# Kernel optimization log

Hardware: AMD Instinct MI355X
Metric: run time of the kernel (lower is better)

The kernel has to match this reference:

```python
import jax, jax.numpy as jnp
import numpy as np

N, IN_F, OUT_F, HEADS = 50000, 128, 16, 4
HC = OUT_F * HEADS  # 64
E = 800000
BN_EPS = 1e-5
NEG_SLOPE = 0.2


def setup_inputs() -> dict:
    key = jax.random.key(0)
    ks = jax.random.split(key, 9)
    x = jax.random.normal(ks[0], (N, IN_F), dtype=jnp.float32)
    edge_index = jax.random.randint(ks[1], (2, E), 0, N, dtype=jnp.int64)
    W = jax.random.normal(ks[2], (IN_F, HC), dtype=jnp.float32) * (1.0 / np.sqrt(IN_F))
    a_src = jax.random.normal(ks[3], (HEADS, OUT_F), dtype=jnp.float32) * 0.1
    a_dst = jax.random.normal(ks[4], (HEADS, OUT_F), dtype=jnp.float32) * 0.1
    bias = jax.random.normal(ks[5], (HC,), dtype=jnp.float32) * 0.01
    gamma = jnp.ones((HC,), dtype=jnp.float32) + 0.1 * jax.random.normal(ks[6], (HC,), dtype=jnp.float32)
    beta = 0.1 * jax.random.normal(ks[7], (HC,), dtype=jnp.float32)
    W_res = jax.random.normal(ks[8], (IN_F, HC), dtype=jnp.float32) * (1.0 / np.sqrt(IN_F))
    return {"x": x, "edge_index": edge_index, "W": W, "a_src": a_src,
            "a_dst": a_dst, "bias": bias, "gamma": gamma, "beta": beta, "W_res": W_res}


def reference(x, edge_index, W, a_src, a_dst, bias, gamma, beta, W_res):
    n = x.shape[0]
    # GATConv adds self-loops by default
    loops = jnp.tile(jnp.arange(n, dtype=edge_index.dtype)[None, :], (2, 1))
    ei = jnp.concatenate([edge_index, loops], axis=1)
    src, dst = ei[0], ei[1]

    h = (x @ W).reshape(n, HEADS, OUT_F)  # [N,H,C]
    al_s = jnp.einsum('nhc,hc->nh', h, a_src)  # [N,H]
    al_d = jnp.einsum('nhc,hc->nh', h, a_dst)

    e = jax.nn.leaky_relu(al_s[src] + al_d[dst], NEG_SLOPE)  # [E,H]
    # per-destination segment softmax (self-loops guarantee non-empty segments)
    e_max = jax.lax.stop_gradient(jax.ops.segment_max(e, dst, num_segments=n))
    m = jnp.exp(e - e_max[dst])
    denom = jax.ops.segment_sum(m, dst, num_segments=n)  # [N,H]
    alpha = m / denom[dst]  # [E,H]

    # scatter-add weighted source features
    msg = alpha[:, :, None] * h[src]  # [E,H,C]
    out = jax.ops.segment_sum(msg, dst, num_segments=n).reshape(n, HC) + bias

    # BatchNorm (training mode: batch statistics over nodes) then ELU
    mu = out.mean(axis=0)
    var = out.var(axis=0)
    y = (out - mu) * jax.lax.rsqrt(var + BN_EPS) * gamma + beta
    y = jax.nn.elu(y)
    # dropout identity (eval); residual projection since in_feats != H*C
    return y + x @ W_res
```

## Files before the change

kernel.cpp:

```cpp
#include <hip/hip_runtime.h>
#include <hip/hip_bf16.h>

#define NN 50000
#define EE 800000
#define IN_F 128
#define HC 64
#define NEG_SLOPE 0.2f
#define BN_EPS 1e-5f

#define NBKT 196
#define NBLKS 200
#define EPB2 (EE / NBLKS)
#define TOTH (NBKT * NBLKS)
#define GEMM_BLOCKS 512
#define NTILES ((NN + 63) / 64)

typedef __attribute__((ext_vector_type(8))) short short8;
typedef __attribute__((ext_vector_type(4))) float f32x4;

__device__ __forceinline__ ushort f2bf(float f) {
  uint u = __float_as_uint(f);
  uint r = u + 0x7FFF + ((u >> 16) & 1);
  return (ushort)(r >> 16);
}
__device__ __forceinline__ float bf2f(ushort u) {
  return __uint_as_float(((uint)u) << 16);
}

__global__ __launch_bounds__(256) void gemm_mfma_kernel(
    const float* __restrict__ x, const float* __restrict__ W, const float* __restrict__ Wres,
    const float* __restrict__ a_src, const float* __restrict__ a_dst,
    ushort* __restrict__ h, ushort* __restrict__ res,
    float* __restrict__ al_s, float* __restrict__ al_d) {
  __shared__ ushort bs[128 * 128];
  __shared__ ushort xs[64 * 128];

  const int tid = threadIdx.x;

  {
    const int c4 = (tid & 31) * 4;
    const int kb = (tid >> 5) * 16;
    const float* src0 = (c4 < HC) ? (W + c4) : (Wres + (c4 - HC));
    char* base = (char*)bs;
#pragma unroll
    for (int j = 0; j < 8; ++j) {
      int k0 = kb + j * 2;
      float4 fa = *(const float4*)(src0 + (size_t)k0 * HC);
      float4 fb = *(const float4*)(src0 + (size_t)(k0 + 1) * HC);
      uint p0 = (uint)f2bf(fa.x) | ((uint)f2bf(fb.x) << 16);
      uint p1 = (uint)f2bf(fa.y) | ((uint)f2bf(fb.y) << 16);
      uint p2 = (uint)f2bf(fa.z) | ((uint)f2bf(fb.z) << 16);
      uint p3 = (uint)f2bf(fa.w) | ((uint)f2bf(fb.w) << 16);
      *(uint*)(base + (((c4 + 0) * 256 + k0 * 2) ^ (((c4 + 0) & 7) << 4))) = p0;
      *(uint*)(base + (((c4 + 1) * 256 + k0 * 2) ^ (((c4 + 1) & 7) << 4))) = p1;
      *(uint*)(base + (((c4 + 2) * 256 + k0 * 2) ^ (((c4 + 2) & 7) << 4))) = p2;
      *(uint*)(base + (((c4 + 3) * 256 + k0 * 2) ^ (((c4 + 3) & 7) << 4))) = p3;
    }
  }

  const int w = tid >> 6;
  const int l = tid & 63;
  const int lr = l & 15;
  const int lk = (l >> 4) * 8;
  const char* xb = (const char*)xs;
  const char* bb = (const char*)bs;
  const int arow = w * 16 + lr;

  for (int rt = blockIdx.x; rt < NTILES; rt += GEMM_BLOCKS) {
    const int r0 = rt * 64;
    __syncthreads();
    {
      char* base = (char*)xs;
#pragma unroll
      for (int i = 0; i < 8; ++i) {
        int f4 = i * 256 + tid;
        int row = f4 >> 5;
        int kq = (f4 & 31) * 4;
        int gr = r0 + row;
        float4 v = make_float4(0.f, 0.f, 0.f, 0.f);
        if (gr < NN) v = *(const float4*)(x + (size_t)gr * IN_F + kq);
        uint lo = (uint)f2bf(v.x) | ((uint)f2bf(v.y) << 16);
        uint hi = (uint)f2bf(v.z) | ((uint)f2bf(v.w) << 16);
        uint off = (uint)((row * 256 + kq * 2) ^ ((row & 7) << 4));
        *(uint2*)(base + off) = make_uint2(lo, hi);
      }
    }
    __syncthreads();

    f32x4 acc[8];
#pragma unroll
    for (int i = 0; i < 8; ++i) acc[i] = (f32x4){0.f, 0.f, 0.f, 0.f};

#pragma unroll
    for (int ks = 0; ks < 4; ++ks) {
      const int kbase = ks * 32 + lk;
      short8 af = *(const short8*)(xb + ((arow * 256 + kbase * 2) ^ ((arow & 7) << 4)));
#pragma unroll
      for (int ct = 0; ct < 8; ++ct) {
        const int c = ct * 16 + lr;
        short8 bfr = *(const short8*)(bb + ((c * 256 + kbase * 2) ^ ((c & 7) << 4)));
        acc[ct] = __builtin_amdgcn_mfma_f32_16x16x32_bf16(af, bfr, acc[ct], 0, 0, 0);
      }
    }

    const int rb = r0 + w * 16;
#pragma unroll
    for (int ct = 0; ct < 8; ++ct) {
#pragma unroll
      for (int r = 0; r < 4; ++r) {
        int gr = rb + (l >> 4) * 4 + r;
        if (gr < NN) {
          if (ct < 4) h[(size_t)gr * HC + ct * 16 + lr] = f2bf(acc[ct][r]);
          else        res[(size_t)gr * HC + (ct - 4) * 16 + lr] = f2bf(acc[ct][r]);
        }
      }
    }

    float myS[4] = {0.f, 0.f, 0.f, 0.f};
    float myD[4] = {0.f, 0.f, 0.f, 0.f};
#pragma unroll
    for (int ct = 0; ct < 4; ++ct) {
      float asv = a_src[ct * 16 + lr];
      float adv = a_dst[ct * 16 + lr];
#pragma unroll
      for (int r = 0; r < 4; ++r) {
        float ps = acc[ct][r] * asv;
        float pd = acc[ct][r] * adv;
        ps += __shfl_xor(ps, 1); ps += __shfl_xor(ps, 2); ps += __shfl_xor(ps, 4); ps += __shfl_xor(ps, 8);
        pd += __shfl_xor(pd, 1); pd += __shfl_xor(pd, 2); pd += __shfl_xor(pd, 4); pd += __shfl_xor(pd, 8);
        if (lr == ct) { myS[r] = ps; myD[r] = pd; }
      }
    }
    if (lr < 4) {
#pragma unroll
      for (int r = 0; r < 4; ++r) {
        int gr = rb + (l >> 4) * 4 + r;
        if (gr < NN) {
          al_s[gr * 4 + lr] = myS[r];
          al_d[gr * 4 + lr] = myD[r];
        }
      }
    }
  }
}

__global__ __launch_bounds__(256) void histB_kernel(const int* __restrict__ dst,
                                                    int* __restrict__ histmat,
                                                    float* __restrict__ sums) {
  __shared__ int lh[NBKT];
  const int tid = threadIdx.x;
  if (blockIdx.x == 0 && tid < 32)
    ((float4*)sums)[tid] = make_float4(0.f, 0.f, 0.f, 0.f);
  for (int i = tid; i < NBKT; i += 256) lh[i] = 0;
  __syncthreads();
  const int4* d4 = (const int4*)(dst + blockIdx.x * EPB2);
  for (int p = tid; p < EPB2 / 4; p += 256) {
    int4 d = d4[p];
    atomicAdd(&lh[d.x >> 8], 1);
    atomicAdd(&lh[d.y >> 8], 1);
    atomicAdd(&lh[d.z >> 8], 1);
    atomicAdd(&lh[d.w >> 8], 1);
  }
  __syncthreads();
  for (int i = tid; i < NBKT; i += 256) histmat[i * NBLKS + blockIdx.x] = lh[i];
}

__global__ __launch_bounds__(256) void scanB_kernel(const int* __restrict__ histmat,
                                                    int* __restrict__ histabs,
                                                    int* __restrict__ bucket_base) {
  const int b = blockIdx.x;
  const int t = threadIdx.x;
  const int lane = t & 63;
  const int wv = t >> 6;
  int part = 0;
  for (int i = t; i < b * NBLKS; i += 256) part += histmat[i];
#pragma unroll
  for (int off = 1; off < 64; off <<= 1) part += __shfl_xor(part, off);
  __shared__ int ws1[4];
  if (lane == 0) ws1[wv] = part;
  __syncthreads();
  const int prefix = ws1[0] + ws1[1] + ws1[2] + ws1[3];
  int v = (t < NBLKS) ? histmat[b * NBLKS + t] : 0;
  int incl = v;
#pragma unroll
  for (int off = 1; off < 64; off <<= 1) {
    int tt = __shfl_up(incl, off);
    if (lane >= off) incl += tt;
  }
  __shared__ int ws2[4];
  if (lane == 63) ws2[wv] = incl;
  __syncthreads();
  int woff = 0;
  for (int w = 0; w < wv; ++w) woff += ws2[w];
  if (t < NBLKS) histabs[b * NBLKS + t] = prefix + woff + incl - v;
  if (t == 0) bucket_base[b] = prefix;
  if (b == NBKT - 1 && t == 0) bucket_base[NBKT] = EE;
}

__global__ __launch_bounds__(256) void placeB_kernel(const int* __restrict__ src,
                                                     const int* __restrict__ dst,
                                                     const int* __restrict__ histabs,
                                                     uint* __restrict__ pairs) {
  __shared__ int cur[NBKT];
  const int tid = threadIdx.x;
  for (int i = tid; i < NBKT; i += 256) cur[i] = histabs[i * NBLKS + blockIdx.x];
  __syncthreads();
  const int4* s4 = (const int4*)(src + blockIdx.x * EPB2);
  const int4* d4 = (const int4*)(dst + blockIdx.x * EPB2);
  for (int p = tid; p < EPB2 / 4; p += 256) {
    int4 d = d4[p];
    int4 s = s4[p];
    int q;
    q = atomicAdd(&cur[d.x >> 8], 1); pairs[q] = ((uint)(d.x & 255) << 16) | (uint)s.x;
    q = atomicAdd(&cur[d.y >> 8], 1); pairs[q] = ((uint)(d.y & 255) << 16) | (uint)s.y;
    q = atomicAdd(&cur[d.z >> 8], 1); pairs[q] = ((uint)(d.z & 255) << 16) | (uint)s.z;
    q = atomicAdd(&cur[d.w >> 8], 1); pairs[q] = ((uint)(d.w & 255) << 16) | (uint)s.w;
  }
}

__global__ __launch_bounds__(256) void bscatter_kernel(const uint* __restrict__ pairs,
                                                       const int* __restrict__ bucket_base,
                                                       int* __restrict__ row_ptr,
                                                       int* __restrict__ col) {
  __shared__ int cnt[256];
  __shared__ int wsum[4];
  const int b = blockIdx.x;
  const int tid = threadIdx.x;
  cnt[tid] = 0;
  __syncthreads();
  const int lo = bucket_base[b];
  const int hi = bucket_base[b + 1];
  for (int i = lo + tid; i < hi; i += 256)
    atomicAdd(&cnt[(pairs[i] >> 16) & 255], 1);
  __syncthreads();
  const int lane = tid & 63;
  const int wv = tid >> 6;
  const int v = cnt[tid];
  int incl = v;
#pragma unroll
  for (int off = 1; off < 64; off <<= 1) {
    int t = __shfl_up(incl, off);
    if (lane >= off) incl += t;
  }
  if (lane == 63) wsum[wv] = incl;
  __syncthreads();
  int woff = 0;
  for (int w = 0; w < wv; ++w) woff += wsum[w];
  const int excl = lo + woff + incl - v;
  __syncthreads();
  cnt[tid] = excl;
  const int node = (b << 8) + tid;
  if (node < NN) row_ptr[node] = excl;
  if (b == NBKT - 1 && tid == 255) row_ptr[NN] = EE;
  __syncthreads();
  for (int i = lo + tid; i < hi; i += 256) {
    uint u = pairs[i];
    int d = (u >> 16) & 255;
    int p = atomicAdd(&cnt[d], 1);
    col[p] = (int)(u & 0xFFFFu);
  }
}

__global__ __launch_bounds__(256) void node_kernel(
    const ushort* __restrict__ h, const float* __restrict__ al_s, const float* __restrict__ al_d,
    const int* __restrict__ row_ptr, const int* __restrict__ col,
    ushort* __restrict__ out_pre) {
  const int node = blockIdx.x * 4 + (threadIdx.x >> 6);
  const int lane = threadIdx.x & 63;
  const int head = lane >> 4;
  const int hdA = lane & 3;
  const int elA = lane >> 2;

  const float aldB = al_d[(uint)node * 4u + head];
  const float aldA = al_d[(uint)node * 4u + hdA];

  float e0 = al_s[(uint)node * 4u + head] + aldB;
  e0 = e0 > 0.f ? e0 : NEG_SLOPE * e0;
  float m = __expf(e0);
  float denom = m;
  float acc = m * bf2f(h[((uint)node << 6) + lane]);

  const int beg = row_ptr[node];
  const int end = row_ptr[node + 1];
  for (int idx = beg; idx < end; idx += 16) {
    const int j = idx + elA;
    const uint sA = (uint)col[j < end ? j : beg];
    float ee = al_s[sA * 4u + hdA] + aldA;
    ee = ee > 0.f ? ee : NEG_SLOPE * ee;
    const float mmA = (j < end) ? __expf(ee) : 0.f;
    uint ss[16];
#pragma unroll
    for (int e = 0; e < 16; ++e) ss[e] = (uint)__shfl((int)sA, e * 4);
    float hv[16];
#pragma unroll
    for (int e = 0; e < 16; ++e) hv[e] = bf2f(h[(ss[e] << 6) + lane]);
    float mm[16];
#pragma unroll
    for (int e = 0; e < 16; ++e) mm[e] = __shfl(mmA, e * 4 + head);
#pragma unroll
    for (int e = 0; e < 16; ++e) {
      denom += mm[e];
      acc = fmaf(mm[e], hv[e], acc);
    }
  }
  out_pre[((uint)node << 6) + lane] = f2bf(acc / denom);
}

__global__ __launch_bounds__(256) void stats_kernel(const uint* __restrict__ out_pre_u,
                                                    float* __restrict__ sums) {
  const int tid = threadIdx.x;
  const int c2 = tid & 31;
  const int rg = tid >> 5;
  float s0 = 0.f, s1 = 0.f, q0 = 0.f, q1 = 0.f;
  for (int r = blockIdx.x * 8 + rg; r < NN; r += gridDim.x * 8) {
    uint u = out_pre_u[((uint)r << 5) + c2];
    float v0 = bf2f((ushort)(u & 0xFFFFu));
    float v1 = bf2f((ushort)(u >> 16));
    s0 += v0; s1 += v1;
    q0 = fmaf(v0, v0, q0); q1 = fmaf(v1, v1, q1);
  }
  __shared__ float l0[256], l1[256], l2[256], l3[256];
  l0[tid] = s0; l1[tid] = s1; l2[tid] = q0; l3[tid] = q1;
  __syncthreads();
  if (tid < 32) {
    float a0 = 0.f, a1 = 0.f, a2 = 0.f, a3 = 0.f;
#pragma unroll
    for (int g = 0; g < 8; ++g) {
      a0 += l0[g * 32 + tid]; a1 += l1[g * 32 + tid];
      a2 += l2[g * 32 + tid]; a3 += l3[g * 32 + tid];
    }
    atomicAdd(&sums[tid * 2], a0);
    atomicAdd(&sums[tid * 2 + 1], a1);
    atomicAdd(&sums[64 + tid * 2], a2);
    atomicAdd(&sums[64 + tid * 2 + 1], a3);
  }
}

__global__ __launch_bounds__(256) void final_kernel(
    const uint* __restrict__ out_pre_u, const uint* __restrict__ res_u,
    const float* __restrict__ sums, const float* __restrict__ gamma,
    const float* __restrict__ beta, float* __restrict__ out) {
  const int i = blockIdx.x * 256 + threadIdx.x;
  const int c4 = (i & 15) * 4;
  const float inv_n = 1.0f / (float)NN;
  uint2 op = *(const uint2*)&out_pre_u[(size_t)i * 2];
  uint2 rs = *(const uint2*)&res_u[(size_t)i * 2];
  float4 g4 = *(const float4*)&gamma[c4];
  float4 b4 = *(const float4*)&beta[c4];
  float pv[4] = { bf2f((ushort)(op.x & 0xFFFFu)), bf2f((ushort)(op.x >> 16)),
                  bf2f((ushort)(op.y & 0xFFFFu)), bf2f((ushort)(op.y >> 16)) };
  float rv[4] = { bf2f((ushort)(rs.x & 0xFFFFu)), bf2f((ushort)(rs.x >> 16)),
                  bf2f((ushort)(rs.y & 0xFFFFu)), bf2f((ushort)(rs.y >> 16)) };
  float gg[4] = { g4.x, g4.y, g4.z, g4.w };
  float bb[4] = { b4.x, b4.y, b4.z, b4.w };
  float4 o;
  float* po = &o.x;
#pragma unroll
  for (int k = 0; k < 4; ++k) {
    int c = c4 + k;
    float mu = sums[c] * inv_n;
    float var = sums[64 + c] * inv_n - mu * mu;
    float rinv = rsqrtf(var + BN_EPS);
    float v = (pv[k] - mu) * rinv * gg[k] + bb[k];
    v = v > 0.f ? v : (__expf(v) - 1.0f);
    po[k] = v + rv[k];
  }
  *(float4*)&out[(size_t)i * 4] = o;
}

extern "C" void kernel_launch(void* const* d_in, const int* in_sizes, int n_in,
                              void* d_out, int out_size, void* d_ws, size_t ws_size,
                              hipStream_t stream) {
  const float* x     = (const float*)d_in[0];
  const int*   ei    = (const int*)d_in[1];
  const float* W     = (const float*)d_in[2];
  const float* a_src = (const float*)d_in[3];
  const float* a_dst = (const float*)d_in[4];
  const float* gamma = (const float*)d_in[6];
  const float* beta  = (const float*)d_in[7];
  const float* Wres  = (const float*)d_in[8];
  float* out = (float*)d_out;

  char* ws = (char*)d_ws;
  ushort* h        = (ushort*)ws; ws += (size_t)NN * HC * 2;
  ushort* resb     = (ushort*)ws; ws += (size_t)NN * HC * 2;
  ushort* out_pre  = (ushort*)ws; ws += (size_t)NN * HC * 2;
  float* al_s      = (float*)ws;  ws += (size_t)NN * 4 * 4;
  float* al_d      = (float*)ws;  ws += (size_t)NN * 4 * 4;
  float* sums      = (float*)ws;  ws += 128 * 4;
  int*   row_ptr   = (int*)ws;    ws += (size_t)(NN + 1) * 4;
  int*   histmat   = (int*)ws;    ws += (size_t)TOTH * 4;
  int*   histabs   = (int*)ws;    ws += (size_t)TOTH * 4;
  int*   bucket_base = (int*)ws;  ws += (NBKT + 1) * 4;
  uint*  pairs     = (uint*)ws;   ws += (size_t)EE * 4;
  int*   col       = (int*)ws;    ws += (size_t)EE * 4;

  gemm_mfma_kernel<<<GEMM_BLOCKS, 256, 0, stream>>>(x, W, Wres, a_src, a_dst,
                                                    h, resb, al_s, al_d);
  histB_kernel<<<NBLKS, 256, 0, stream>>>(ei + EE, histmat, sums);
  scanB_kernel<<<NBKT, 256, 0, stream>>>(histmat, histabs, bucket_base);
  placeB_kernel<<<NBLKS, 256, 0, stream>>>(ei, ei + EE, histabs, pairs);
  bscatter_kernel<<<NBKT, 256, 0, stream>>>(pairs, bucket_base, row_ptr, col);
  node_kernel<<<NN / 4, 256, 0, stream>>>(h, al_s, al_d, row_ptr, col, out_pre);
  stats_kernel<<<256, 256, 0, stream>>>((const uint*)out_pre, sums);
  final_kernel<<<NN * HC / 1024, 256, 0, stream>>>((const uint*)out_pre, (const uint*)resb,
                                                   sums, gamma, beta, out);
}
```

Before: 122.6 us.

## Fuse bucket scan into placement kernel and retune GEMM grid size

New measurement: 105.2 us. 14.2% less time.

```diff
diff --git a/kernel.cpp b/kernel.cpp
--- a/kernel.cpp
+++ b/kernel.cpp
@@ -12,7 +12,7 @@
 #define NBLKS 200
 #define EPB2 (EE / NBLKS)
 #define TOTH (NBKT * NBLKS)
-#define GEMM_BLOCKS 512
+#define GEMM_BLOCKS 391
 #define NTILES ((NN + 63) / 64)
 
 typedef __attribute__((ext_vector_type(8))) short short8;
@@ -165,48 +165,47 @@
   for (int i = tid; i < NBKT; i += 256) histmat[i * NBLKS + blockIdx.x] = lh[i];
 }
 
-__global__ __launch_bounds__(256) void scanB_kernel(const int* __restrict__ histmat,
-                                                    int* __restrict__ histabs,
-                                                    int* __restrict__ bucket_base) {
+__global__ __launch_bounds__(256) void placeB_kernel(const int* __restrict__ src,
+                                                     const int* __restrict__ dst,
+                                                     const int* __restrict__ histmat,
+                                                     uint* __restrict__ pairs,
+                                                     int* __restrict__ bucket_base) {
+  __shared__ int cur[NBKT];
+  __shared__ int ws2[4];
   const int b = blockIdx.x;
-  const int t = threadIdx.x;
-  const int lane = t & 63;
-  const int wv = t >> 6;
-  int part = 0;
-  for (int i = t; i < b * NBLKS; i += 256) part += histmat[i];
-#pragma unroll
-  for (int off = 1; off < 64; off <<= 1) part += __shfl_xor(part, off);
-  __shared__ int ws1[4];
-  if (lane == 0) ws1[wv] = part;
-  __syncthreads();
-  const int prefix = ws1[0] + ws1[1] + ws1[2] + ws1[3];
-  int v = (t < NBLKS) ? histmat[b * NBLKS + t] : 0;
-  int incl = v;
+  const int tid = threadIdx.x;
+  const int lane = tid & 63;
+  const int wv = tid >> 6;
+
+  int rowsum = 0, colpart = 0;
+  if (tid < NBKT) {
+    const int* row = histmat + tid * NBLKS;
+    for (int c = 0; c < NBLKS; ++c) {
+      int v = row[c];
+      rowsum += v;
+      colpart += (c < b) ? v : 0;
+    }
+  }
+  int incl = rowsum;
 #pragma unroll
   for (int off = 1; off < 64; off <<= 1) {
-    int tt = __shfl_up(incl, off);
-    if (lane >= off) incl += tt;
-  }
-  __shared__ int ws2[4];
+    int t = __shfl_up(incl, off);
+    if (lane >= off) incl += t;
+  }
   if (lane == 63) ws2[wv] = incl;
   __syncthreads();
   int woff = 0;
   for (int w = 0; w < wv; ++w) woff += ws2[w];
-  if (t < NBLKS) histabs[b * NBLKS + t] = prefix + woff + incl - v;
-  if (t == 0) bucket_base[b] = prefix;
-  if (b == NBKT - 1 && t == 0) bucket_base[NBKT] = EE;
-}
-
-__global__ __launch_bounds__(256) void placeB_kernel(const int* __restrict__ src,
-                                                     const int* __restrict__ dst,
-                                                     const int* __restrict__ histabs,
-                                                     uint* __restrict__ pairs) {
-  __shared__ int cur[NBKT];
-  const int tid = threadIdx.x;
-  for (int i = tid; i < NBKT; i += 256) cur[i] = histabs[i * NBLKS + blockIdx.x];
-  __syncthreads();
-  const int4* s4 = (const int4*)(src + blockIdx.x * EPB2);
-  const int4* d4 = (const int4*)(dst + blockIdx.x * EPB2);
+  const int excl = woff + incl - rowsum;
+  if (tid < NBKT) {
+    cur[tid] = excl + colpart;
+    if (b == 0) bucket_base[tid] = excl;
+  }
+  if (b == 0 && tid == 0) bucket_base[NBKT] = EE;
+  __syncthreads();
+
+  const int4* s4 = (const int4*)(src + b * EPB2);
+  const int4* d4 = (const int4*)(dst + b * EPB2);
   for (int p = tid; p < EPB2 / 4; p += 256) {
     int4 d = d4[p];
     int4 s = s4[p];
@@ -390,7 +389,6 @@
   float* sums      = (float*)ws;  ws += 128 * 4;
   int*   row_ptr   = (int*)ws;    ws += (size_t)(NN + 1) * 4;
   int*   histmat   = (int*)ws;    ws += (size_t)TOTH * 4;
-  int*   histabs   = (int*)ws;    ws += (size_t)TOTH * 4;
   int*   bucket_base = (int*)ws;  ws += (NBKT + 1) * 4;
   uint*  pairs     = (uint*)ws;   ws += (size_t)EE * 4;
   int*   col       = (int*)ws;    ws += (size_t)EE * 4;
@@ -398,8 +396,7 @@
   gemm_mfma_kernel<<<GEMM_BLOCKS, 256, 0, stream>>>(x, W, Wres, a_src, a_dst,
                                                     h, resb, al_s, al_d);
   histB_kernel<<<NBLKS, 256, 0, stream>>>(ei + EE, histmat, sums);
-  scanB_kernel<<<NBKT, 256, 0, stream>>>(histmat, histabs, bucket_base);
-  placeB_kernel<<<NBLKS, 256, 0, stream>>>(ei, ei + EE, histabs, pairs);
+  placeB_kernel<<<NBLKS, 256, 0, stream>>>(ei, ei + EE, histmat, pairs, bucket_base);
   bscatter_kernel<<<NBKT, 256, 0, stream>>>(pairs, bucket_base, row_ptr, col);
   node_kernel<<<NN / 4, 256, 0, stream>>>(h, al_s, al_d, row_ptr, col, out_pre);
   stats_kernel<<<256, 256, 0, stream>>>((const uint*)out_pre, sums);
```
